# Performance work log

Measured on AMD Instinct MI355X. Metric: run time of the kernel, lower is better.

The kernel has to match this reference:

```python
import jax, jax.numpy as jnp
import numpy as np

B, S, D, H, SE, DE, DFF = 4, 1024, 1024, 16, 77, 768, 4096


def _ln(x, g, b, eps=1e-5):
    mu = jnp.mean(x, axis=-1, keepdims=True)
    var = jnp.mean((x - mu) ** 2, axis=-1, keepdims=True)
    return (x - mu) * jax.lax.rsqrt(var + eps) * g + b


def _split_heads(x, heads):
    b, s, d = x.shape
    return x.reshape(b, s, heads, d // heads).transpose(0, 2, 1, 3)  # b h s hd


def _attn(q, k, v, heads):
    # memory_efficient_attention equivalent: softmax(q k^T * scale) v, per head
    q, k, v = _split_heads(q, heads), _split_heads(k, heads), _split_heads(v, heads)
    scale = q.shape[-1] ** -0.5
    scores = jnp.einsum('bhqd,bhkd->bhqk', q, k) * scale
    probs = jax.nn.softmax(scores, axis=-1)
    o = jnp.einsum('bhqk,bhkd->bhqd', probs, v)
    b, h, s, hd = o.shape
    return o.transpose(0, 2, 1, 3).reshape(b, s, h * hd)


def _geglu_ff(x, w1, b1, w2, b2):
    proj = x @ w1 + b1
    a, gate = jnp.split(proj, 2, axis=-1)
    return (a * jax.nn.gelu(gate)) @ w2 + b2


def _forward(h1, h2, enc, wq, wk, wv, wqc, wo, bo, ln1g, ln1b, ln2g, ln2b,
             w2q, w2k, w2v, w2o, b2o, wff1, bff1, wff2, bff2):
    # norm1
    n1 = _ln(h1, ln1g[0], ln1b[0])
    n2 = _ln(h2, ln1g[1], ln1b[1])
    # dual-stream uni-direction attention (self + cross with swapped K/V)
    q1, k1, v1, q1c = n1 @ wq[0], n1 @ wk[0], n1 @ wv[0], n1 @ wqc[0]
    q2, k2, v2, q2c = n2 @ wq[1], n2 @ wk[1], n2 @ wv[1], n2 @ wqc[1]
    a1 = _attn(q1, k1, v1, H) + _attn(q1c, k2, v2, H)
    a2 = _attn(q2, k2, v2, H) + _attn(q2c, k1, v1, H)
    a1 = a1 @ wo[0] + bo[0]
    a2 = a2 @ wo[1] + bo[1]
    h1 = h1 + a1
    h2 = h2 + a2
    # cross attention to encoder states (attn2)
    n1 = _ln(h1, ln2g[0], ln2b[0])
    n2 = _ln(h2, ln2g[1], ln2b[1])
    c1 = _attn(n1 @ w2q[0], enc @ w2k[0], enc @ w2v[0], H) @ w2o[0] + b2o[0]
    c2 = _attn(n2 @ w2q[1], enc @ w2k[1], enc @ w2v[1], H) @ w2o[1] + b2o[1]
    h1 = h1 + c1
    h2 = h2 + c2
    # feed-forward (GEGLU), applied to norm2 output exactly as in source
    h1 = h1 + _geglu_ff(n1, wff1[0], bff1[0], wff2[0], bff2[0])
    h2 = h2 + _geglu_ff(n2, wff1[1], bff1[1], wff2[1], bff2[1])
    return (h1, h2)


def setup_inputs() -> dict:
    key = jax.random.key(0)
    ks = jax.random.split(key, 16)
    f = lambda k, shp: jax.random.normal(k, shp, jnp.float32) * 0.02
    return {
        'h1': jax.random.normal(ks[0], (B, S, D), jnp.float32),
        'h2': jax.random.normal(ks[1], (B, S, D), jnp.float32),
        'enc': jax.random.normal(ks[2], (B, SE, DE), jnp.float32),
        'wq': f(ks[3], (2, D, D)), 'wk': f(ks[4], (2, D, D)),
        'wv': f(ks[5], (2, D, D)), 'wqc': f(ks[6], (2, D, D)),
        'wo': f(ks[7], (2, D, D)), 'bo': jnp.zeros((2, D), jnp.float32),
        'ln1g': jnp.ones((2, D), jnp.float32), 'ln1b': jnp.zeros((2, D), jnp.float32),
        'ln2g': jnp.ones((2, D), jnp.float32), 'ln2b': jnp.zeros((2, D), jnp.float32),
        'w2q': f(ks[8], (2, D, D)), 'w2k': f(ks[9], (2, DE, D)),
        'w2v': f(ks[10], (2, DE, D)), 'w2o': f(ks[11], (2, D, D)),
        'b2o': jnp.zeros((2, D), jnp.float32),
        'wff1': f(ks[12], (2, D, 2 * DFF)), 'bff1': jnp.zeros((2, 2 * DFF), jnp.float32),
        'wff2': f(ks[13], (2, DFF, D)), 'bff2': jnp.zeros((2, D), jnp.float32),
    }


def reference(h1, h2, enc, wq, wk, wv, wqc, wo, bo, ln1g, ln1b, ln2g, ln2b,
              w2q, w2k, w2v, w2o, b2o, wff1, bff1, wff2, bff2):
    return _forward(h1, h2, enc, wq, wk, wv, wqc, wo, bo, ln1g, ln1b, ln2g, ln2b,
                    w2q, w2k, w2v, w2o, b2o, wff1, bff1, wff2, bff2)
```

## Files before the change

### kernel.cpp

```cpp
#include <hip/hip_runtime.h>

typedef unsigned short u16;
typedef short v8s __attribute__((ext_vector_type(8)));
typedef float v4f __attribute__((ext_vector_type(4)));

__device__ __forceinline__ float bf2f(u16 u) {
  union { unsigned u; float f; } c; c.u = ((unsigned)u) << 16; return c.f;
}
__device__ __forceinline__ u16 f2bf(float x) {
  union { float f; unsigned u; } c; c.f = x;
  unsigned r = c.u + 0x7fffu + ((c.u >> 16) & 1u);
  return (u16)(r >> 16);
}
__device__ __forceinline__ v4f vzero() { v4f z; z[0]=0.f; z[1]=0.f; z[2]=0.f; z[3]=0.f; return z; }
__device__ __forceinline__ v4f mfma16(v8s a, v8s b, v4f c) {
  return __builtin_amdgcn_mfma_f32_16x16x32_bf16(a, b, c, 0, 0, 0);
}
__device__ __forceinline__ void async_lds16(const void* g, void* l) {
  __builtin_amdgcn_global_load_lds((__attribute__((address_space(1))) void*)g,
                                   (__attribute__((address_space(3))) void*)l, 16, 0, 0);
}
__device__ __forceinline__ float gelu_f(float x) {
  return 0.5f * x * (1.f + tanhf(0.7978845608028654f * (x + 0.044715f * x * x * x)));
}

__global__ void detect_k(const unsigned* __restrict__ p, unsigned* __restrict__ flag) {
  if (threadIdx.x == 0) {
    flag[0] = (p[0] == 0x3F803F80u) ? 1u : 0u;
    flag[1] = 0u;
  }
}

__global__ __launch_bounds__(256) void cvt_k(const unsigned* __restrict__ flag,
    const void* __restrict__ src, u16* __restrict__ dst, int n) {
  int i = (blockIdx.x * 256 + threadIdx.x) * 8;
  if (i >= n) return;
  if (*flag) {
    *(uint4*)(dst + i) = *(const uint4*)((const u16*)src + i);
  } else {
    const float* s = (const float*)src + i;
    #pragma unroll
    for (int j = 0; j < 8; ++j) dst[i + j] = f2bf(s[j]);
  }
}

__global__ __launch_bounds__(256) void tr_k(const unsigned* __restrict__ flag,
    const void* __restrict__ in, u16* __restrict__ out, int R, int C, long outZS) {
  __shared__ u16 tile[32][33];
  size_t zin = (size_t)blockIdx.z * R * C;
  size_t zout = (size_t)blockIdx.z * outZS;
  int c0 = blockIdx.x * 32, r0 = blockIdx.y * 32;
  int tx = threadIdx.x & 31, ty = threadIdx.x >> 5;
  unsigned isbf = *flag;
  const u16* inb = (const u16*)in + zin;
  const float* inf = (const float*)in + zin;
  #pragma unroll
  for (int i = ty; i < 32; i += 8) {
    size_t idx = (size_t)(r0 + i) * C + c0 + tx;
    tile[i][tx] = isbf ? inb[idx] : f2bf(inf[idx]);
  }
  __syncthreads();
  out += zout;
  #pragma unroll
  for (int i = ty; i < 32; i += 8) out[(size_t)(c0 + i) * R + r0 + tx] = tile[tx][i];
}

__global__ __launch_bounds__(256) void ln_k(const unsigned* __restrict__ flag,
    const void* __restrict__ src0, const void* __restrict__ src1,
    const u16* __restrict__ gw, const u16* __restrict__ bw, u16* __restrict__ out) {
  int z = blockIdx.y;
  const void* src = z ? src1 : src0;
  out += (size_t)z * 4194304; gw += z * 1024; bw += z * 1024;
  int row = blockIdx.x, t = threadIdx.x;
  unsigned isbf = *flag;
  float4 v;
  if (isbf) {
    uint2 d = ((const uint2*)((const u16*)src + (size_t)row * 1024))[t];
    v.x = bf2f((u16)(d.x & 0xffffu)); v.y = bf2f((u16)(d.x >> 16));
    v.z = bf2f((u16)(d.y & 0xffffu)); v.w = bf2f((u16)(d.y >> 16));
  } else {
    v = ((const float4*)((const float*)src + (size_t)row * 1024))[t];
  }
  float s = v.x + v.y + v.z + v.w;
  float s2 = v.x * v.x + v.y * v.y + v.z * v.z + v.w * v.w;
  #pragma unroll
  for (int o = 32; o; o >>= 1) { s += __shfl_down(s, o); s2 += __shfl_down(s2, o); }
  __shared__ float red[8];
  int w = t >> 6;
  if ((t & 63) == 0) { red[w] = s; red[4 + w] = s2; }
  __syncthreads();
  if (t == 0) {
    red[0] = red[0] + red[1] + red[2] + red[3];
    red[4] = red[4] + red[5] + red[6] + red[7];
  }
  __syncthreads();
  float mu = red[0] * (1.f / 1024.f);
  float var = red[4] * (1.f / 1024.f) - mu * mu;
  float rstd = rsqrtf(var + 1e-5f);
  int c = t * 4;
  float xs[4] = { v.x, v.y, v.z, v.w };
  #pragma unroll
  for (int j = 0; j < 4; ++j) {
    float g = bf2f(gw[c + j]), bb = bf2f(bw[c + j]);
    out[(size_t)row * 1024 + c + j] = f2bf((xs[j] - mu) * rstd * g + bb);
  }
}

template<int EPI>
__global__ __launch_bounds__(256, 2) void gemm_bt(
    const u16* __restrict__ A, const u16* __restrict__ Bt,
    int M, int N, int K, int lda, int ldb, int ldc,
    const u16* __restrict__ bias, const u16* aux,
    float* __restrict__ resF, void* __restrict__ outB,
    long zsA, long zsB, long zsC, int zsBias,
    const void* rin0, const void* rin1,
    const unsigned* __restrict__ flagp)
{
  int z = blockIdx.z;
  A += (size_t)z * zsA;
  Bt += (size_t)z * zsB;
  size_t zc = (size_t)z * zsC;
  unsigned isbf = 0;
  if (EPI == 4 || EPI == 5) isbf = *flagp;
  const void* rin = (EPI == 5) ? (z ? rin1 : rin0) : nullptr;
  __shared__ alignas(16) u16 As[128 * 64];
  __shared__ alignas(16) u16 Bs[128 * 64];
  int tid = threadIdx.x;
  int lane = tid & 63, wave = tid >> 6;
  int l15 = lane & 15, l4 = lane >> 4;
  int wm = wave & 1, wn = wave >> 1;
  int m0 = blockIdx.x * 128, n0 = blockIdx.y * 128;
  v4f acc[4][4];
  #pragma unroll
  for (int i = 0; i < 4; ++i)
    #pragma unroll
    for (int j = 0; j < 4; ++j) acc[i][j] = vzero();

  for (int k0 = 0; k0 < K; k0 += 64) {
    #pragma unroll
    for (int it = 0; it < 4; ++it) {
      int sidx = it * 256 + tid;
      int r = sidx >> 3, cs = (sidx & 7) * 8;
      int ra = m0 + r; if (ra > M - 1) ra = M - 1;
      async_lds16(A + (size_t)ra * lda + k0 + cs, As + (size_t)(it * 256 + wave * 64) * 8);
      async_lds16(Bt + (size_t)(n0 + r) * ldb + k0 + cs, Bs + (size_t)(it * 256 + wave * 64) * 8);
    }
    __syncthreads();
    #pragma unroll
    for (int ks = 0; ks < 2; ++ks) {
      v8s af[4], bfr[4];
      #pragma unroll
      for (int i = 0; i < 4; ++i) {
        af[i]  = *(const v8s*)(As + (wm * 64 + i * 16 + l15) * 64 + ks * 32 + l4 * 8);
        bfr[i] = *(const v8s*)(Bs + (wn * 64 + i * 16 + l15) * 64 + ks * 32 + l4 * 8);
      }
      #pragma unroll
      for (int i = 0; i < 4; ++i)
        #pragma unroll
        for (int j = 0; j < 4; ++j)
          acc[i][j] = mfma16(af[i], bfr[j], acc[i][j]);
    }
    __syncthreads();
  }
  #pragma unroll
  for (int mt = 0; mt < 4; ++mt) {
    #pragma unroll
    for (int r = 0; r < 4; ++r) {
      int gr = m0 + wm * 64 + mt * 16 + l4 * 4 + r;
      if (gr >= M) continue;
      size_t ri = (size_t)gr * ldc;
      size_t ro = zc + ri;
      #pragma unroll
      for (int nt = 0; nt < 4; ++nt) {
        int gc = n0 + wn * 64 + nt * 16 + l15;
        float v = acc[mt][nt][r];
        if (bias) v += bf2f(bias[(size_t)z * zsBias + gc]);
        if (EPI == 0) ((u16*)outB)[ro + gc] = f2bf(v);
        else if (EPI == 1) ((u16*)outB)[ro + gc] = f2bf(gelu_f(v));
        else if (EPI == 2) ((u16*)outB)[ro + gc] = f2bf(v * bf2f(aux[ro + gc]));
        else if (EPI == 3) resF[ro + gc] += v;
        else if (EPI == 5) {
          float h = isbf ? bf2f(((const u16*)rin)[ri + gc]) : ((const float*)rin)[ri + gc];
          resF[ro + gc] = h + v;
        } else {
          float o = resF[ro + gc] + v;
          if (isbf) ((u16*)outB)[ro + gc] = f2bf(o);
          else ((float*)outB)[ro + gc] = o;
        }
      }
    }
  }
}

__global__ __launch_bounds__(256, 2) void flash_self_k(
    const u16* __restrict__ qkv, u16* __restrict__ O)
{
  __shared__ alignas(16) u16 Ksh[128 * 64];
  __shared__ alignas(16) unsigned VshT[64 * 68];
  __shared__ alignas(16) u16 Psh[4 * 16 * 40];
  int tid = threadIdx.x, lane = tid & 63, wave = tid >> 6;
  int l15 = lane & 15, l4 = lane >> 4;
  int h = blockIdx.y;
  int strm = blockIdx.z >> 2, b = blockIdx.z & 3;
  const size_t ZS = 16777216;
  const size_t BS = 4194304;
  int q0 = blockIdx.x * 64 + wave * 16;
  u16* pw = Psh + wave * 640;
  v4f res[4];
  #pragma unroll
  for (int i = 0; i < 4; ++i) res[i] = vzero();

  for (int sg = 0; sg < 2; ++sg) {
    int qcol = sg ? 3072 : 0;
    int ks = sg ? (strm ^ 1) : strm;
    const u16* Qb = qkv + (size_t)strm * ZS + (size_t)b * BS + qcol + h * 64;
    const u16* Kb = qkv + (size_t)ks * ZS + (size_t)b * BS + 1024 + h * 64;
    const u16* Vb = Kb + 1024;
    v8s qf0 = *(const v8s*)(Qb + (size_t)(q0 + l15) * 4096 + l4 * 8);
    v8s qf1 = *(const v8s*)(Qb + (size_t)(q0 + l15) * 4096 + l4 * 8 + 32);
    v4f oacc[4];
    #pragma unroll
    for (int i = 0; i < 4; ++i) oacc[i] = vzero();
    float mrun[4], lrun[4];
    #pragma unroll
    for (int r = 0; r < 4; ++r) { mrun[r] = -1e30f; lrun[r] = 0.f; }

    for (int c0 = 0; c0 < 1024; c0 += 128) {
      #pragma unroll
      for (int it = 0; it < 4; ++it) {
        int sidx = it * 256 + tid;
        int key = sidx >> 3, ds8 = (sidx & 7) * 8;
        async_lds16(Kb + (size_t)(c0 + key) * 4096 + ds8, Ksh + (size_t)(it * 256 + wave * 64) * 8);
      }
      #pragma unroll
      for (int it = 0; it < 2; ++it) {
        int tt = it * 256 + tid;
        int kp = tt & 63, dsg = tt >> 6;
        v8s v0 = *(const v8s*)(Vb + (size_t)(c0 + kp * 2) * 4096 + dsg * 8);
        v8s v1 = *(const v8s*)(Vb + (size_t)(c0 + kp * 2 + 1) * 4096 + dsg * 8);
        #pragma unroll
        for (int j = 0; j < 8; ++j) {
          unsigned pk = (unsigned)(u16)v0[j] | ((unsigned)(u16)v1[j] << 16);
          VshT[(dsg * 8 + j) * 68 + kp] = pk;
        }
      }
      __syncthreads();
      #pragma unroll
      for (int g = 0; g < 4; ++g) {
        v4f s0 = vzero(), s1 = vzero();
        {
          v8s b0 = *(const v8s*)(Ksh + (g * 32 + l15) * 64 + l4 * 8);
          v8s b1 = *(const v8s*)(Ksh + (g * 32 + 16 + l15) * 64 + l4 * 8);
          s0 = mfma16(qf0, b0, s0);
          s1 = mfma16(qf0, b1, s1);
          b0 = *(const v8s*)(Ksh + (g * 32 + l15) * 64 + 32 + l4 * 8);
          b1 = *(const v8s*)(Ksh + (g * 32 + 16 + l15) * 64 + 32 + l4 * 8);
          s0 = mfma16(qf1, b0, s0);
          s1 = mfma16(qf1, b1, s1);
        }
        float x0[4], x1[4], tm[4];
        #pragma unroll
        for (int r = 0; r < 4; ++r) {
          x0[r] = s0[r] * 0.125f;
          x1[r] = s1[r] * 0.125f;
          tm[r] = fmaxf(x0[r], x1[r]);
        }
        #pragma unroll
        for (int o = 8; o; o >>= 1)
          #pragma unroll
          for (int r = 0; r < 4; ++r) tm[r] = fmaxf(tm[r], __shfl_xor(tm[r], o));
        float alpha[4], rs[4], p0[4], p1[4];
        #pragma unroll
        for (int r = 0; r < 4; ++r) {
          float mn = fmaxf(mrun[r], tm[r]);
          alpha[r] = __expf(mrun[r] - mn);
          mrun[r] = mn;
          p0[r] = __expf(x0[r] - mn);
          p1[r] = __expf(x1[r] - mn);
          rs[r] = p0[r] + p1[r];
        }
        #pragma unroll
        for (int o = 8; o; o >>= 1)
          #pragma unroll
          for (int r = 0; r < 4; ++r) rs[r] += __shfl_xor(rs[r], o);
        #pragma unroll
        for (int r = 0; r < 4; ++r) {
          lrun[r] = lrun[r] * alpha[r] + rs[r];
          oacc[0][r] *= alpha[r]; oacc[1][r] *= alpha[r];
          oacc[2][r] *= alpha[r]; oacc[3][r] *= alpha[r];
        }
        #pragma unroll
        for (int r = 0; r < 4; ++r) {
          int row = l4 * 4 + r;
          pw[row * 40 + l15]      = f2bf(p0[r]);
          pw[row * 40 + 16 + l15] = f2bf(p1[r]);
        }
        v8s pa = *(const v8s*)(pw + l15 * 40 + l4 * 8);
        #pragma unroll
        for (int nt = 0; nt < 4; ++nt) {
          v8s vb = *(const v8s*)((const u16*)VshT + (nt * 16 + l15) * 136 + g * 32 + l4 * 8);
          oacc[nt] = mfma16(pa, vb, oacc[nt]);
        }
      }
      __syncthreads();
    }
    #pragma unroll
    for (int r = 0; r < 4; ++r) {
      float inv = 1.f / lrun[r];
      #pragma unroll
      for (int nt = 0; nt < 4; ++nt) res[nt][r] += oacc[nt][r] * inv;
    }
  }
  #pragma unroll
  for (int nt = 0; nt < 4; ++nt) {
    #pragma unroll
    for (int r = 0; r < 4; ++r) {
      int gq = q0 + l4 * 4 + r;
      size_t oi = (size_t)strm * BS + ((size_t)b * 1024 + gq) * 1024 + h * 64 + nt * 16 + l15;
      O[oi] = f2bf(res[nt][r]);
    }
  }
}

__global__ __launch_bounds__(256, 2) void flash_cross_k(
    const u16* __restrict__ Q, const u16* __restrict__ KV, u16* __restrict__ O)
{
  __shared__ alignas(16) u16 Ksh[128 * 64];
  __shared__ alignas(16) unsigned VshT[64 * 68];
  __shared__ alignas(16) u16 Psh[4 * 16 * 40];
  int tid = threadIdx.x, lane = tid & 63, wave = tid >> 6;
  int l15 = lane & 15, l4 = lane >> 4;
  int h = blockIdx.y;
  int strm = blockIdx.z >> 2, b = blockIdx.z & 3;
  const u16* Qb = Q + (size_t)strm * 4194304 + (size_t)b * 1048576 + h * 64;
  const u16* Kb = KV + (size_t)strm * 630784 + (size_t)b * 157696 + h * 64;
  const u16* Vb = Kb + 1024;
  int q0 = blockIdx.x * 64 + wave * 16;
  u16* pw = Psh + wave * 640;
  v8s qf0 = *(const v8s*)(Qb + (size_t)(q0 + l15) * 1024 + l4 * 8);
  v8s qf1 = *(const v8s*)(Qb + (size_t)(q0 + l15) * 1024 + l4 * 8 + 32);
  v4f oacc[4];
  #pragma unroll
  for (int i = 0; i < 4; ++i) oacc[i] = vzero();
  float mrun[4], lrun[4];
  #pragma unroll
  for (int r = 0; r < 4; ++r) { mrun[r] = -1e30f; lrun[r] = 0.f; }

  #pragma unroll
  for (int it = 0; it < 4; ++it) {
    int sidx = it * 256 + tid;
    int key = sidx >> 3, ds8 = (sidx & 7) * 8;
    int gk = key > 76 ? 76 : key;
    async_lds16(Kb + (size_t)gk * 2048 + ds8, Ksh + (size_t)(it * 256 + wave * 64) * 8);
  }
  #pragma unroll
  for (int it = 0; it < 2; ++it) {
    int tt = it * 256 + tid;
    int kp = tt & 63, dsg = tt >> 6;
    int gk0 = kp * 2, gk1 = kp * 2 + 1;
    if (gk0 > 76) gk0 = 76;
    if (gk1 > 76) gk1 = 76;
    v8s v0 = *(const v8s*)(Vb + (size_t)gk0 * 2048 + dsg * 8);
    v8s v1 = *(const v8s*)(Vb + (size_t)gk1 * 2048 + dsg * 8);
    #pragma unroll
    for (int j = 0; j < 8; ++j) {
      unsigned pk = (unsigned)(u16)v0[j] | ((unsigned)(u16)v1[j] << 16);
      VshT[(dsg * 8 + j) * 68 + kp] = pk;
    }
  }
  __syncthreads();
  #pragma unroll
  for (int g = 0; g < 4; ++g) {
    v4f s0 = vzero(), s1 = vzero();
    {
      v8s b0 = *(const v8s*)(Ksh + (g * 32 + l15) * 64 + l4 * 8);
      v8s b1 = *(const v8s*)(Ksh + (g * 32 + 16 + l15) * 64 + l4 * 8);
      s0 = mfma16(qf0, b0, s0);
      s1 = mfma16(qf0, b1, s1);
      b0 = *(const v8s*)(Ksh + (g * 32 + l15) * 64 + 32 + l4 * 8);
      b1 = *(const v8s*)(Ksh + (g * 32 + 16 + l15) * 64 + 32 + l4 * 8);
      s0 = mfma16(qf1, b0, s0);
      s1 = mfma16(qf1, b1, s1);
    }
    int key0 = g * 32 + l15;
    bool ok0 = key0 < 77, ok1 = (key0 + 16) < 77;
    float x0[4], x1[4], tm[4];
    #pragma unroll
    for (int r = 0; r < 4; ++r) {
      x0[r] = ok0 ? s0[r] * 0.125f : -1e30f;
      x1[r] = ok1 ? s1[r] * 0.125f : -1e30f;
      tm[r] = fmaxf(x0[r], x1[r]);
    }
    #pragma unroll
    for (int o = 8; o; o >>= 1)
      #pragma unroll
      for (int r = 0; r < 4; ++r) tm[r] = fmaxf(tm[r], __shfl_xor(tm[r], o));
    float alpha[4], rs[4], p0[4], p1[4];
    #pragma unroll
    for (int r = 0; r < 4; ++r) {
      float mn = fmaxf(mrun[r], tm[r]);
      alpha[r] = __expf(mrun[r] - mn);
      mrun[r] = mn;
      p0[r] = __expf(x0[r] - mn);
      p1[r] = __expf(x1[r] - mn);
      rs[r] = p0[r] + p1[r];
    }
    #pragma unroll
    for (int o = 8; o; o >>= 1)
      #pragma unroll
      for (int r = 0; r < 4; ++r) rs[r] += __shfl_xor(rs[r], o);
    #pragma unroll
    for (int r = 0; r < 4; ++r) {
      lrun[r] = lrun[r] * alpha[r] + rs[r];
      oacc[0][r] *= alpha[r]; oacc[1][r] *= alpha[r];
      oacc[2][r] *= alpha[r]; oacc[3][r] *= alpha[r];
    }
    #pragma unroll
    for (int r = 0; r < 4; ++r) {
      int row = l4 * 4 + r;
      pw[row * 40 + l15]      = f2bf(p0[r]);
      pw[row * 40 + 16 + l15] = f2bf(p1[r]);
    }
    v8s pa = *(const v8s*)(pw + l15 * 40 + l4 * 8);
    #pragma unroll
    for (int nt = 0; nt < 4; ++nt) {
      v8s vb = *(const v8s*)((const u16*)VshT + (nt * 16 + l15) * 136 + g * 32 + l4 * 8);
      oacc[nt] = mfma16(pa, vb, oacc[nt]);
    }
  }
  #pragma unroll
  for (int nt = 0; nt < 4; ++nt) {
    #pragma unroll
    for (int r = 0; r < 4; ++r) {
      int gq = q0 + l4 * 4 + r;
      size_t oi = (size_t)strm * 4194304 + ((size_t)b * 1024 + gq) * 1024 + h * 64 + nt * 16 + l15;
      O[oi] = f2bf(oacc[nt][r] / lrun[r]);
    }
  }
}

extern "C" void kernel_launch(void* const* d_in, const int* in_sizes, int n_in,
                              void* d_out, int out_size, void* d_ws, size_t ws_size,
                              hipStream_t stream)
{
  (void)in_sizes; (void)n_in; (void)out_size;
  const void* h1   = d_in[0];
  const void* h2   = d_in[1];
  const void* enc  = d_in[2];
  const void* wq   = d_in[3];
  const void* wk   = d_in[4];
  const void* wv   = d_in[5];
  const void* wqc  = d_in[6];
  const void* wo   = d_in[7];
  const void* bo   = d_in[8];
  const void* ln1g = d_in[9];
  const void* ln1b = d_in[10];
  const void* ln2g = d_in[11];
  const void* ln2b = d_in[12];
  const void* w2q  = d_in[13];
  const void* w2k  = d_in[14];
  const void* w2v  = d_in[15];
  const void* w2o  = d_in[16];
  const void* b2o  = d_in[17];
  const void* wff1 = d_in[18];
  const void* bff1 = d_in[19];
  const void* wff2 = d_in[20];
  const void* bff2 = d_in[21];

  const size_t S1 = 4194304;
  const size_t W1 = 1048576;
  const size_t QS = 16777216;
  const size_t NE = 236544;

  char* base = (char*)d_ws;
  size_t off = 0;
  auto AL = [&](size_t n) { size_t r = off; off += (n + 255) & ~(size_t)255; return r; };
  size_t o_flag   = AL(256);
  size_t o_pb     = AL(30720 * 2);
  size_t o_encB   = AL(NE * 2);
  size_t o_wqkvT  = AL(2 * 4 * W1 * 2);
  size_t o_woT    = AL(2 * W1 * 2);
  size_t o_w2qT   = AL(2 * W1 * 2);
  size_t o_w2oT   = AL(2 * W1 * 2);
  size_t o_w2kvT  = AL(2 * 2048 * 768 * 2);
  size_t o_wff1T  = AL(2 * 8192 * 1024 * 2);
  size_t o_wff2T  = AL(2 * 4096 * 1024 * 2);
  size_t o_hw     = AL(2 * S1 * 4);
  size_t o_n      = AL(2 * S1 * 2);
  size_t o_qkv    = AL(2 * QS * 2);
  size_t o_ab     = AL(2 * S1 * 2);
  if (ws_size < off) return;

  unsigned* flagp = (unsigned*)(base + o_flag);
  const unsigned* zerop = flagp + 1;
  u16* pb = (u16*)(base + o_pb);
  u16* boB   = pb + 0;
  u16* b2oB  = pb + 2048;
  u16* ln1gB = pb + 4096;
  u16* ln1bB = pb + 6144;
  u16* ln2gB = pb + 8192;
  u16* ln2bB = pb + 10240;
  u16* bff2B = pb + 12288;
  u16* bff1B = pb + 14336;
  u16* encB  = (u16*)(base + o_encB);
  u16* wqkvT = (u16*)(base + o_wqkvT);
  u16* woT   = (u16*)(base + o_woT);
  u16* w2qT  = (u16*)(base + o_w2qT);
  u16* w2oT  = (u16*)(base + o_w2oT);
  u16* w2kvT = (u16*)(base + o_w2kvT);
  u16* wff1T = (u16*)(base + o_wff1T);
  u16* wff2T = (u16*)(base + o_wff2T);
  float* hw  = (float*)(base + o_hw);
  u16* n1    = (u16*)(base + o_n);
  u16* qkv   = (u16*)(base + o_qkv);
  u16* a1b   = (u16*)(base + o_ab);
  u16* q1x   = qkv;
  u16* c1b   = qkv + 2 * S1;
  u16* kencv = qkv + 4 * S1;
  u16* gelu  = qkv;

  auto tr = [&](const void* ip, u16* op, int R, int C, long outZS) {
    dim3 g(C / 32, R / 32, 2);
    tr_k<<<g, 256, 0, stream>>>(flagp, ip, op, R, C, outZS);
  };
  auto cvt = [&](const void* ip, u16* op, int n) {
    cvt_k<<<(n / 8 + 255) / 256, 256, 0, stream>>>(flagp, ip, op, n);
  };
  auto gemm = [&](int epi, const u16* Ap, const u16* Bp, int M, int N, int K,
                  int lda, int ldb, int ldc, const u16* bias, const u16* aux,
                  float* resF, void* oB, int nz, long zsA, long zsB, long zsC, int zsBias,
                  const void* rin0, const void* rin1) {
    dim3 g((M + 127) / 128, N / 128, nz);
    switch (epi) {
      case 0: gemm_bt<0><<<g, 256, 0, stream>>>(Ap, Bp, M, N, K, lda, ldb, ldc, bias, aux, resF, oB, zsA, zsB, zsC, zsBias, rin0, rin1, flagp); break;
      case 1: gemm_bt<1><<<g, 256, 0, stream>>>(Ap, Bp, M, N, K, lda, ldb, ldc, bias, aux, resF, oB, zsA, zsB, zsC, zsBias, rin0, rin1, flagp); break;
      case 2: gemm_bt<2><<<g, 256, 0, stream>>>(Ap, Bp, M, N, K, lda, ldb, ldc, bias, aux, resF, oB, zsA, zsB, zsC, zsBias, rin0, rin1, flagp); break;
      case 3: gemm_bt<3><<<g, 256, 0, stream>>>(Ap, Bp, M, N, K, lda, ldb, ldc, bias, aux, resF, oB, zsA, zsB, zsC, zsBias, rin0, rin1, flagp); break;
      case 4: gemm_bt<4><<<g, 256, 0, stream>>>(Ap, Bp, M, N, K, lda, ldb, ldc, bias, aux, resF, oB, zsA, zsB, zsC, zsBias, rin0, rin1, flagp); break;
      default: gemm_bt<5><<<g, 256, 0, stream>>>(Ap, Bp, M, N, K, lda, ldb, ldc, bias, aux, resF, oB, zsA, zsB, zsC, zsBias, rin0, rin1, flagp); break;
    }
  };

  detect_k<<<1, 64, 0, stream>>>((const unsigned*)ln1g, flagp);
  cvt(bo, boB, 2048);     cvt(b2o, b2oB, 2048);
  cvt(ln1g, ln1gB, 2048); cvt(ln1b, ln1bB, 2048);
  cvt(ln2g, ln2gB, 2048); cvt(ln2b, ln2bB, 2048);
  cvt(bff2, bff2B, 2048); cvt(bff1, bff1B, 16384);
  cvt(enc, encB, (int)NE);
  tr(wq,  wqkvT + 0 * W1, 1024, 1024, 4 * (long)W1);
  tr(wk,  wqkvT + 1 * W1, 1024, 1024, 4 * (long)W1);
  tr(wv,  wqkvT + 2 * W1, 1024, 1024, 4 * (long)W1);
  tr(wqc, wqkvT + 3 * W1, 1024, 1024, 4 * (long)W1);
  tr(wo,  woT,  1024, 1024, (long)W1);
  tr(w2q, w2qT, 1024, 1024, (long)W1);
  tr(w2o, w2oT, 1024, 1024, (long)W1);
  tr(w2k, w2kvT + 0,          768, 1024, 2048L * 768);
  tr(w2v, w2kvT + 1024 * 768, 768, 1024, 2048L * 768);
  tr(wff1, wff1T, 1024, 8192, 8192L * 1024);
  tr(wff2, wff2T, 4096, 1024, 4096L * 1024);
  ln_k<<<dim3(4096, 2), 256, 0, stream>>>(flagp, h1, h2, ln1gB, ln1bB, n1);
  gemm(0, n1, wqkvT, 4096, 4096, 1024, 1024, 1024, 4096, nullptr, nullptr, nullptr, qkv,
       2, (long)S1, 4 * (long)W1, (long)QS, 0, nullptr, nullptr);
  flash_self_k<<<dim3(16, 16, 8), 256, 0, stream>>>(qkv, a1b);
  gemm(5, a1b, woT, 4096, 1024, 1024, 1024, 1024, 1024, boB, nullptr, hw, nullptr,
       2, (long)S1, (long)W1, (long)S1, 1024, h1, h2);
  ln_k<<<dim3(4096, 2), 256, 0, stream>>>(zerop, hw, hw + S1, ln2gB, ln2bB, n1);
  gemm(0, n1, w2qT, 4096, 1024, 1024, 1024, 1024, 1024, nullptr, nullptr, nullptr, q1x,
       2, (long)S1, (long)W1, (long)S1, 0, nullptr, nullptr);
  gemm(0, encB, w2kvT, 308, 2048, 768, 768, 768, 2048, nullptr, nullptr, nullptr, kencv,
       2, 0, 2048L * 768, 308L * 2048, 0, nullptr, nullptr);
  flash_cross_k<<<dim3(16, 16, 8), 256, 0, stream>>>(q1x, kencv, c1b);
  gemm(3, c1b, w2oT, 4096, 1024, 1024, 1024, 1024, 1024, b2oB, nullptr, hw, nullptr,
       2, (long)S1, (long)W1, (long)S1, 1024, nullptr, nullptr);
  gemm(1, n1, wff1T + 4096 * 1024, 4096, 4096, 1024, 1024, 1024, 4096,
       bff1B + 4096, nullptr, nullptr, gelu, 2, (long)S1, 8192L * 1024, (long)QS, 8192,
       nullptr, nullptr);
  gemm(2, n1, wff1T, 4096, 4096, 1024, 1024, 1024, 4096,
       bff1B, gelu, nullptr, gelu, 2, (long)S1, 8192L * 1024, (long)QS, 8192,
       nullptr, nullptr);
  gemm(4, gelu, wff2T, 4096, 1024, 4096, 4096, 4096, 1024,
       bff2B, nullptr, hw, d_out, 2, (long)QS, 4096L * 1024, (long)S1, 1024,
       nullptr, nullptr);
}
```

Before: 1.370 ms.

## Pre-transpose V, swizzle LDS tiles, and process whole key chunks per softmax step

A separate kernel transposes V into a per-head d-major buffer, which reuses the n1 scratch area. This lets flash_self_k load V into LDS with async global-to-LDS copies instead of register repacking. K, V and P tiles in LDS use XOR swizzles to avoid bank conflicts. The online softmax now runs once per 128-key chunk instead of once per 32-key group, and MFMA phases are wrapped in setprio. The cross kernel gets the same P swizzle and single-pass softmax. The cost is an extra transpose kernel launch plus a round trip of V through global memory, and more LDS per block.

Result: faster. 1.222 ms (-10.8%).

```diff
diff --git a/kernel.cpp b/kernel.cpp
--- a/kernel.cpp
+++ b/kernel.cpp
@@ -63,6 +63,22 @@
   out += zout;
   #pragma unroll
   for (int i = ty; i < 32; i += 8) out[(size_t)(c0 + i) * R + r0 + tx] = tile[tx][i];
+}
+
+__global__ __launch_bounds__(256) void vtr_k(const u16* __restrict__ in, u16* __restrict__ out) {
+  __shared__ u16 tile[32][33];
+  int z = blockIdx.z >> 2, b = blockIdx.z & 3;
+  const u16* ip = in + (size_t)z * 16777216 + (size_t)b * 4194304 + 2048;
+  u16* op = out + (size_t)z * 4194304 + (size_t)b * 1048576;
+  int k0 = blockIdx.x * 32, d0 = blockIdx.y * 32;
+  int tx = threadIdx.x & 31, ty = threadIdx.x >> 5;
+  #pragma unroll
+  for (int i = ty; i < 32; i += 8)
+    tile[i][tx] = ip[(size_t)(k0 + i) * 4096 + d0 + tx];
+  __syncthreads();
+  #pragma unroll
+  for (int i = ty; i < 32; i += 8)
+    op[(size_t)(d0 + i) * 1024 + k0 + tx] = tile[tx][i];
 }
 
 __global__ __launch_bounds__(256) void ln_k(const unsigned* __restrict__ flag,
@@ -193,11 +209,11 @@
 }
 
 __global__ __launch_bounds__(256, 2) void flash_self_k(
-    const u16* __restrict__ qkv, u16* __restrict__ O)
+    const u16* __restrict__ qkv, const u16* __restrict__ Vt, u16* __restrict__ O)
 {
   __shared__ alignas(16) u16 Ksh[128 * 64];
-  __shared__ alignas(16) unsigned VshT[64 * 68];
-  __shared__ alignas(16) u16 Psh[4 * 16 * 40];
+  __shared__ alignas(16) u16 Vsh[64 * 128];
+  __shared__ alignas(16) u16 Psh[4][16 * 128];
   int tid = threadIdx.x, lane = tid & 63, wave = tid >> 6;
   int l15 = lane & 15, l4 = lane >> 4;
   int h = blockIdx.y;
@@ -205,17 +221,18 @@
   const size_t ZS = 16777216;
   const size_t BS = 4194304;
   int q0 = blockIdx.x * 64 + wave * 16;
-  u16* pw = Psh + wave * 640;
+  u16* pw = Psh[wave];
+  int swz = l15 & 7;
   v4f res[4];
   #pragma unroll
   for (int i = 0; i < 4; ++i) res[i] = vzero();
 
   for (int sg = 0; sg < 2; ++sg) {
     int qcol = sg ? 3072 : 0;
-    int ks = sg ? (strm ^ 1) : strm;
+    int ksrc = sg ? (strm ^ 1) : strm;
     const u16* Qb = qkv + (size_t)strm * ZS + (size_t)b * BS + qcol + h * 64;
-    const u16* Kb = qkv + (size_t)ks * ZS + (size_t)b * BS + 1024 + h * 64;
-    const u16* Vb = Kb + 1024;
+    const u16* Kb = qkv + (size_t)ksrc * ZS + (size_t)b * BS + 1024 + h * 64;
+    const u16* Vb = Vt + (size_t)ksrc * BS + (size_t)b * 1048576 + h * 65536;
     v8s qf0 = *(const v8s*)(Qb + (size_t)(q0 + l15) * 4096 + l4 * 8);
     v8s qf1 = *(const v8s*)(Qb + (size_t)(q0 + l15) * 4096 + l4 * 8 + 32);
     v4f oacc[4];
@@ -229,79 +246,80 @@
       #pragma unroll
       for (int it = 0; it < 4; ++it) {
         int sidx = it * 256 + tid;
-        int key = sidx >> 3, ds8 = (sidx & 7) * 8;
-        async_lds16(Kb + (size_t)(c0 + key) * 4096 + ds8, Ksh + (size_t)(it * 256 + wave * 64) * 8);
-      }
-      #pragma unroll
-      for (int it = 0; it < 2; ++it) {
-        int tt = it * 256 + tid;
-        int kp = tt & 63, dsg = tt >> 6;
-        v8s v0 = *(const v8s*)(Vb + (size_t)(c0 + kp * 2) * 4096 + dsg * 8);
-        v8s v1 = *(const v8s*)(Vb + (size_t)(c0 + kp * 2 + 1) * 4096 + dsg * 8);
+        int r = sidx >> 3, c = sidx & 7;
+        async_lds16(Kb + (size_t)(c0 + r) * 4096 + ((c ^ (r & 7)) * 8),
+                    Ksh + (size_t)(it * 256 + wave * 64) * 8);
+      }
+      #pragma unroll
+      for (int it = 0; it < 4; ++it) {
+        int sidx = it * 256 + tid;
+        int d = sidx >> 4, c = sidx & 15;
+        async_lds16(Vb + (size_t)d * 1024 + c0 + ((c ^ (d & 15)) * 8),
+                    Vsh + (size_t)(it * 256 + wave * 64) * 8);
+      }
+      __syncthreads();
+      v4f s[4][2];
+      #pragma unroll
+      for (int g = 0; g < 4; ++g) { s[g][0] = vzero(); s[g][1] = vzero(); }
+      __builtin_amdgcn_s_setprio(1);
+      #pragma unroll
+      for (int g = 0; g < 4; ++g) {
+        int rb0 = (g * 32 + l15) * 64, rb1 = rb0 + 16 * 64;
+        v8s k00 = *(const v8s*)(Ksh + rb0 + ((l4 ^ swz) * 8));
+        v8s k10 = *(const v8s*)(Ksh + rb1 + ((l4 ^ swz) * 8));
+        v8s k01 = *(const v8s*)(Ksh + rb0 + (((4 + l4) ^ swz) * 8));
+        v8s k11 = *(const v8s*)(Ksh + rb1 + (((4 + l4) ^ swz) * 8));
+        s[g][0] = mfma16(qf0, k00, s[g][0]);
+        s[g][1] = mfma16(qf0, k10, s[g][1]);
+        s[g][0] = mfma16(qf1, k01, s[g][0]);
+        s[g][1] = mfma16(qf1, k11, s[g][1]);
+      }
+      __builtin_amdgcn_s_setprio(0);
+      float alpha[4];
+      #pragma unroll
+      for (int r = 0; r < 4; ++r) {
+        int row = l4 * 4 + r;
+        float x[8];
+        #pragma unroll
+        for (int g = 0; g < 4; ++g) {
+          x[2 * g]     = s[g][0][r] * 0.125f;
+          x[2 * g + 1] = s[g][1][r] * 0.125f;
+        }
+        float tm = fmaxf(fmaxf(fmaxf(x[0], x[1]), fmaxf(x[2], x[3])),
+                         fmaxf(fmaxf(x[4], x[5]), fmaxf(x[6], x[7])));
+        #pragma unroll
+        for (int o = 8; o; o >>= 1) tm = fmaxf(tm, __shfl_xor(tm, o));
+        float mn = fmaxf(mrun[r], tm);
+        alpha[r] = __expf(mrun[r] - mn);
+        mrun[r] = mn;
+        float rs = 0.f;
         #pragma unroll
         for (int j = 0; j < 8; ++j) {
-          unsigned pk = (unsigned)(u16)v0[j] | ((unsigned)(u16)v1[j] << 16);
-          VshT[(dsg * 8 + j) * 68 + kp] = pk;
+          float p = __expf(x[j] - mn);
+          rs += p;
+          int col = (j >> 1) * 32 + (j & 1) * 16 + l15;
+          pw[row * 128 + (((col >> 3) ^ row) * 8) + (col & 7)] = f2bf(p);
         }
-      }
-      __syncthreads();
+        #pragma unroll
+        for (int o = 8; o; o >>= 1) rs += __shfl_xor(rs, o);
+        lrun[r] = lrun[r] * alpha[r] + rs;
+      }
+      #pragma unroll
+      for (int nt = 0; nt < 4; ++nt)
+        #pragma unroll
+        for (int r = 0; r < 4; ++r) oacc[nt][r] *= alpha[r];
+      __builtin_amdgcn_s_setprio(1);
       #pragma unroll
       for (int g = 0; g < 4; ++g) {
-        v4f s0 = vzero(), s1 = vzero();
-        {
-          v8s b0 = *(const v8s*)(Ksh + (g * 32 + l15) * 64 + l4 * 8);
-          v8s b1 = *(const v8s*)(Ksh + (g * 32 + 16 + l15) * 64 + l4 * 8);
-          s0 = mfma16(qf0, b0, s0);
-          s1 = mfma16(qf0, b1, s1);
-          b0 = *(const v8s*)(Ksh + (g * 32 + l15) * 64 + 32 + l4 * 8);
-          b1 = *(const v8s*)(Ksh + (g * 32 + 16 + l15) * 64 + 32 + l4 * 8);
-          s0 = mfma16(qf1, b0, s0);
-          s1 = mfma16(qf1, b1, s1);
-        }
-        float x0[4], x1[4], tm[4];
-        #pragma unroll
-        for (int r = 0; r < 4; ++r) {
-          x0[r] = s0[r] * 0.125f;
-          x1[r] = s1[r] * 0.125f;
-          tm[r] = fmaxf(x0[r], x1[r]);
-        }
-        #pragma unroll
-        for (int o = 8; o; o >>= 1)
-          #pragma unroll
-          for (int r = 0; r < 4; ++r) tm[r] = fmaxf(tm[r], __shfl_xor(tm[r], o));
-        float alpha[4], rs[4], p0[4], p1[4];
-        #pragma unroll
-        for (int r = 0; r < 4; ++r) {
-          float mn = fmaxf(mrun[r], tm[r]);
-          alpha[r] = __expf(mrun[r] - mn);
-          mrun[r] = mn;
-          p0[r] = __expf(x0[r] - mn);
-          p1[r] = __expf(x1[r] - mn);
-          rs[r] = p0[r] + p1[r];
-        }
-        #pragma unroll
-        for (int o = 8; o; o >>= 1)
-          #pragma unroll
-          for (int r = 0; r < 4; ++r) rs[r] += __shfl_xor(rs[r], o);
-        #pragma unroll
-        for (int r = 0; r < 4; ++r) {
-          lrun[r] = lrun[r] * alpha[r] + rs[r];
-          oacc[0][r] *= alpha[r]; oacc[1][r] *= alpha[r];
-          oacc[2][r] *= alpha[r]; oacc[3][r] *= alpha[r];
-        }
-        #pragma unroll
-        for (int r = 0; r < 4; ++r) {
-          int row = l4 * 4 + r;
-          pw[row * 40 + l15]      = f2bf(p0[r]);
-          pw[row * 40 + 16 + l15] = f2bf(p1[r]);
-        }
-        v8s pa = *(const v8s*)(pw + l15 * 40 + l4 * 8);
+        v8s pa = *(const v8s*)(pw + l15 * 128 + (((g * 4 + l4) ^ l15) * 8));
         #pragma unroll
         for (int nt = 0; nt < 4; ++nt) {
-          v8s vb = *(const v8s*)((const u16*)VshT + (nt * 16 + l15) * 136 + g * 32 + l4 * 8);
+          int vr = nt * 16 + l15;
+          v8s vb = *(const v8s*)(Vsh + vr * 128 + (((g * 4 + l4) ^ (vr & 15)) * 8));
           oacc[nt] = mfma16(pa, vb, oacc[nt]);
         }
       }
+      __builtin_amdgcn_s_setprio(0);
       __syncthreads();
     }
     #pragma unroll
@@ -327,7 +345,7 @@
 {
   __shared__ alignas(16) u16 Ksh[128 * 64];
   __shared__ alignas(16) unsigned VshT[64 * 68];
-  __shared__ alignas(16) u16 Psh[4 * 16 * 40];
+  __shared__ alignas(16) u16 Psh[4][16 * 128];
   int tid = threadIdx.x, lane = tid & 63, wave = tid >> 6;
   int l15 = lane & 15, l4 = lane >> 4;
   int h = blockIdx.y;
@@ -336,22 +354,18 @@
   const u16* Kb = KV + (size_t)strm * 630784 + (size_t)b * 157696 + h * 64;
   const u16* Vb = Kb + 1024;
   int q0 = blockIdx.x * 64 + wave * 16;
-  u16* pw = Psh + wave * 640;
+  u16* pw = Psh[wave];
+  int swz = l15 & 7;
   v8s qf0 = *(const v8s*)(Qb + (size_t)(q0 + l15) * 1024 + l4 * 8);
   v8s qf1 = *(const v8s*)(Qb + (size_t)(q0 + l15) * 1024 + l4 * 8 + 32);
-  v4f oacc[4];
-  #pragma unroll
-  for (int i = 0; i < 4; ++i) oacc[i] = vzero();
-  float mrun[4], lrun[4];
-  #pragma unroll
-  for (int r = 0; r < 4; ++r) { mrun[r] = -1e30f; lrun[r] = 0.f; }
 
   #pragma unroll
   for (int it = 0; it < 4; ++it) {
     int sidx = it * 256 + tid;
-    int key = sidx >> 3, ds8 = (sidx & 7) * 8;
-    int gk = key > 76 ? 76 : key;
-    async_lds16(Kb + (size_t)gk * 2048 + ds8, Ksh + (size_t)(it * 256 + wave * 64) * 8);
+    int r = sidx >> 3, c = sidx & 7;
+    int gk = r > 76 ? 76 : r;
+    async_lds16(Kb + (size_t)gk * 2048 + ((c ^ (r & 7)) * 8),
+                Ksh + (size_t)(it * 256 + wave * 64) * 8);
   }
   #pragma unroll
   for (int it = 0; it < 2; ++it) {
@@ -369,72 +383,71 @@
     }
   }
   __syncthreads();
+  v4f s[4][2];
+  #pragma unroll
+  for (int g = 0; g < 4; ++g) { s[g][0] = vzero(); s[g][1] = vzero(); }
+  __builtin_amdgcn_s_setprio(1);
   #pragma unroll
   for (int g = 0; g < 4; ++g) {
-    v4f s0 = vzero(), s1 = vzero();
-    {
-      v8s b0 = *(const v8s*)(Ksh + (g * 32 + l15) * 64 + l4 * 8);
-      v8s b1 = *(const v8s*)(Ksh + (g * 32 + 16 + l15) * 64 + l4 * 8);
-      s0 = mfma16(qf0, b0, s0);
-      s1 = mfma16(qf0, b1, s1);
-      b0 = *(const v8s*)(Ksh + (g * 32 + l15) * 64 + 32 + l4 * 8);
-      b1 = *(const v8s*)(Ksh + (g * 32 + 16 + l15) * 64 + 32 + l4 * 8);
-      s0 = mfma16(qf1, b0, s0);
-      s1 = mfma16(qf1, b1, s1);
-    }
-    int key0 = g * 32 + l15;
-    bool ok0 = key0 < 77, ok1 = (key0 + 16) < 77;
-    float x0[4], x1[4], tm[4];
-    #pragma unroll
-    for (int r = 0; r < 4; ++r) {
-      x0[r] = ok0 ? s0[r] * 0.125f : -1e30f;
-      x1[r] = ok1 ? s1[r] * 0.125f : -1e30f;
-      tm[r] = fmaxf(x0[r], x1[r]);
-    }
-    #pragma unroll
-    for (int o = 8; o; o >>= 1)
-      #pragma unroll
-      for (int r = 0; r < 4; ++r) tm[r] = fmaxf(tm[r], __shfl_xor(tm[r], o));
-    float alpha[4], rs[4], p0[4], p1[4];
-    #pragma unroll
-    for (int r = 0; r < 4; ++r) {
-      float mn = fmaxf(mrun[r], tm[r]);
-      alpha[r] = __expf(mrun[r] - mn);
-      mrun[r] = mn;
-      p0[r] = __expf(x0[r] - mn);
-      p1[r] = __expf(x1[r] - mn);
-      rs[r] = p0[r] + p1[r];
-    }
-    #pragma unroll
-    for (int o = 8; o; o >>= 1)
-      #pragma unroll
-      for (int r = 0; r < 4; ++r) rs[r] += __shfl_xor(rs[r], o);
-    #pragma unroll
-    for (int r = 0; r < 4; ++r) {
-      lrun[r] = lrun[r] * alpha[r] + rs[r];
-      oacc[0][r] *= alpha[r]; oacc[1][r] *= alpha[r];
-      oacc[2][r] *= alpha[r]; oacc[3][r] *= alpha[r];
-    }
-    #pragma unroll
-    for (int r = 0; r < 4; ++r) {
-      int row = l4 * 4 + r;
-      pw[row * 40 + l15]      = f2bf(p0[r]);
-      pw[row * 40 + 16 + l15] = f2bf(p1[r]);
-    }
-    v8s pa = *(const v8s*)(pw + l15 * 40 + l4 * 8);
+    int rb0 = (g * 32 + l15) * 64, rb1 = rb0 + 16 * 64;
+    v8s k00 = *(const v8s*)(Ksh + rb0 + ((l4 ^ swz) * 8));
+    v8s k10 = *(const v8s*)(Ksh + rb1 + ((l4 ^ swz) * 8));
+    v8s k01 = *(const v8s*)(Ksh + rb0 + (((4 + l4) ^ swz) * 8));
+    v8s k11 = *(const v8s*)(Ksh + rb1 + (((4 + l4) ^ swz) * 8));
+    s[g][0] = mfma16(qf0, k00, s[g][0]);
+    s[g][1] = mfma16(qf0, k10, s[g][1]);
+    s[g][0] = mfma16(qf1, k01, s[g][0]);
+    s[g][1] = mfma16(qf1, k11, s[g][1]);
+  }
+  __builtin_amdgcn_s_setprio(0);
+  float lsum[4];
+  #pragma unroll
+  for (int r = 0; r < 4; ++r) {
+    int row = l4 * 4 + r;
+    float x[8];
+    #pragma unroll
+    for (int g = 0; g < 4; ++g) {
+      bool ok0 = (g * 32 + l15) < 77, ok1 = (g * 32 + 16 + l15) < 77;
+      x[2 * g]     = ok0 ? s[g][0][r] * 0.125f : -1e30f;
+      x[2 * g + 1] = ok1 ? s[g][1][r] * 0.125f : -1e30f;
+    }
+    float tm = fmaxf(fmaxf(fmaxf(x[0], x[1]), fmaxf(x[2], x[3])),
+                     fmaxf(fmaxf(x[4], x[5]), fmaxf(x[6], x[7])));
+    #pragma unroll
+    for (int o = 8; o; o >>= 1) tm = fmaxf(tm, __shfl_xor(tm, o));
+    float rs = 0.f;
+    #pragma unroll
+    for (int j = 0; j < 8; ++j) {
+      float p = __expf(x[j] - tm);
+      rs += p;
+      int col = (j >> 1) * 32 + (j & 1) * 16 + l15;
+      pw[row * 128 + (((col >> 3) ^ row) * 8) + (col & 7)] = f2bf(p);
+    }
+    #pragma unroll
+    for (int o = 8; o; o >>= 1) rs += __shfl_xor(rs, o);
+    lsum[r] = rs;
+  }
+  v4f oacc[4];
+  #pragma unroll
+  for (int i = 0; i < 4; ++i) oacc[i] = vzero();
+  __builtin_amdgcn_s_setprio(1);
+  #pragma unroll
+  for (int g = 0; g < 4; ++g) {
+    v8s pa = *(const v8s*)(pw + l15 * 128 + (((g * 4 + l4) ^ l15) * 8));
     #pragma unroll
     for (int nt = 0; nt < 4; ++nt) {
       v8s vb = *(const v8s*)((const u16*)VshT + (nt * 16 + l15) * 136 + g * 32 + l4 * 8);
       oacc[nt] = mfma16(pa, vb, oacc[nt]);
     }
   }
+  __builtin_amdgcn_s_setprio(0);
   #pragma unroll
   for (int nt = 0; nt < 4; ++nt) {
     #pragma unroll
     for (int r = 0; r < 4; ++r) {
       int gq = q0 + l4 * 4 + r;
       size_t oi = (size_t)strm * 4194304 + ((size_t)b * 1024 + gq) * 1024 + h * 64 + nt * 16 + l15;
-      O[oi] = f2bf(oacc[nt][r] / lrun[r]);
+      O[oi] = f2bf(oacc[nt][r] / lsum[r]);
     }
   }
 }
@@ -518,6 +531,7 @@
   u16* c1b   = qkv + 2 * S1;
   u16* kencv = qkv + 4 * S1;
   u16* gelu  = qkv;
+  u16* vtb   = n1;
 
   auto tr = [&](const void* ip, u16* op, int R, int C, long outZS) {
     dim3 g(C / 32, R / 32, 2);
@@ -561,7 +575,8 @@
   ln_k<<<dim3(4096, 2), 256, 0, stream>>>(flagp, h1, h2, ln1gB, ln1bB, n1);
   gemm(0, n1, wqkvT, 4096, 4096, 1024, 1024, 1024, 4096, nullptr, nullptr, nullptr, qkv,
        2, (long)S1, 4 * (long)W1, (long)QS, 0, nullptr, nullptr);
-  flash_self_k<<<dim3(16, 16, 8), 256, 0, stream>>>(qkv, a1b);
+  vtr_k<<<dim3(32, 32, 8), 256, 0, stream>>>(qkv, vtb);
+  flash_self_k<<<dim3(16, 16, 8), 256, 0, stream>>>(qkv, vtb, a1b);
   gemm(5, a1b, woT, 4096, 1024, 1024, 1024, 1024, 1024, boB, nullptr, hw, nullptr,
        2, (long)S1, (long)W1, (long)S1, 1024, h1, h2);
   ln_k<<<dim3(4096, 2), 256, 0, stream>>>(zerop, hw, hw + S1, ln2gB, ln2bB, n1);
```
